# Performance work log

Hardware: AMD Instinct MI355X
Metric: run time of the kernel (lower is better)

Reference implementation:

```python
import jax, jax.numpy as jnp
import numpy as np

CUTOFF = 5.0
NIPSIN = 3
NELE = 4        # natomtype
NWAVE = 10      # ntype: radial params per element
NB, NA, NEIGH = 1, 12000, 64
NPAIR = NA * NEIGH
# index_para: maps 12 angular components (3 p + 9 d) to order index 0/1
INDEX_PARA = np.concatenate([np.full(3 ** i, i - 1, dtype=np.int32) for i in range(1, NIPSIN)])
NANG = INDEX_PARA.shape[0]  # 12


def setup_inputs() -> dict:
    key = jax.random.key(0)
    ks = jax.random.split(key, 8)
    coordinates = jax.random.normal(ks[0], (NB, NA, 3), dtype=jnp.float32)
    numatoms = NA
    atom_index = jax.random.randint(ks[1], (2, NB, NPAIR), 0, NA)
    shifts = jax.random.normal(ks[2], (NB, NPAIR, 3), dtype=jnp.float32) * 0.1
    species = jax.random.randint(ks[3], (NB * NA,), 0, NELE)
    rs = jax.random.uniform(ks[4], (NELE, NWAVE), dtype=jnp.float32) * 4.0
    inta = jax.random.uniform(ks[5], (NELE, NWAVE), dtype=jnp.float32) + 0.2
    params = jax.random.uniform(ks[6], (NELE,), dtype=jnp.float32) * 0.5 + 0.5
    return {"coordinates": coordinates, "numatoms": numatoms, "atom_index": atom_index,
            "shifts": shifts, "species": species, "rs": rs, "inta": inta, "params": params}


def _density(coordinates, atom_index, shifts, species, rs, inta):
    nb, na, _ = coordinates.shape
    coords = coordinates.reshape(-1, 3)
    totnatom = coords.shape[0]
    npair = atom_index.shape[2]
    # flatten pair index lists with per-molecule atom offset (faithful for nb=1)
    ai = jnp.transpose(atom_index, (1, 0, 2)).reshape(2, -1)                 # (2, nb*npair)
    off = jnp.broadcast_to((jnp.arange(nb) * na)[:, None], (nb, npair)).reshape(-1)
    idx12 = ai + off[None, :]
    shift_v = shifts.reshape(-1, 3)
    valid = jnp.all(shift_v > -1e9, axis=-1)                                 # padding mask (all True here)
    dist_vec = coords[idx12[0]] - coords[idx12[1]] + shift_v                 # (P,3)
    d = jnp.linalg.norm(dist_vec, axis=-1)                                   # (P,)
    sp = species[idx12[0]]                                                   # (P,)
    # radial Gaussian * cosine cutoff, params gathered per center-atom type
    fcut = 0.5 * (jnp.cos(jnp.pi * jnp.minimum(d / CUTOFF, 1.0)) + 1.0)
    radial = jnp.exp(-10.0 * inta[sp] * jnp.square(d[:, None] - rs[sp])) * fcut[:, None]
    radial = jnp.where(valid[:, None], radial, 0.0)                          # (P, NWAVE)
    # angular outer products of unit vectors: p (3) then d (9)
    u = dist_vec / d[:, None]
    orbs = []
    orb = jnp.ones((u.shape[0], 1), dtype=u.dtype)
    for _ in range(1, NIPSIN):
        orb = (orb[:, :, None] * u[:, None, :]).reshape(u.shape[0], -1)
        orbs.append(orb)
    angular = jnp.concatenate(orbs, axis=1)                                  # (P, NANG)
    # scatter-reduce into per-(atom, neighbor-type) accumulators, then square
    seg = idx12[0] * NELE + sp
    rd = jax.ops.segment_sum(radial, seg, num_segments=totnatom * NELE)
    rd = jnp.square(rd).reshape(totnatom, NELE, NWAVE)
    oa = (angular[:, :, None] * radial[:, None, :]).reshape(u.shape[0], -1)  # (P, NANG*NWAVE)
    ad = jax.ops.segment_sum(oa, seg, num_segments=totnatom * NELE)
    ad = jnp.square(ad).reshape(totnatom, NELE, NANG, NWAVE)
    # contract angular components of the same order (index_para)
    acc = jnp.zeros((totnatom, NELE, NIPSIN - 1, NWAVE), dtype=ad.dtype)
    acc = acc.at[:, :, jnp.asarray(INDEX_PARA), :].add(ad)
    return jnp.concatenate([rd, acc.reshape(totnatom, NELE, -1)], axis=2)    # (T, NELE, 30)


def reference(coordinates, numatoms, atom_index, shifts, species, rs, inta, params):
    density = _density(coordinates, atom_index, shifts, species, rs, inta)
    density_w = density * params[None, :, None]                 # einsum('ijk,j->ijk')
    g = jnp.einsum('ilj,imj->ijlm', density_w, density_w)       # (T, nfeat, NELE, NELE)
    return jnp.sqrt(g).reshape(g.shape[0], g.shape[1], -1).sum(-1)  # (T, nfeat)
```

## Files before the change

### kernel.cpp

```cpp
#include <hip/hip_runtime.h>
#include <math.h>

#define NA 12000
#define NPAIR 768000
#define NWAVE 10
#define BINS 256
#define APB 47
#define BCAP 4096
#define RCAP 3584
#define PPB 3072

__global__ __launch_bounds__(512) void bin_kernel(
        const float* __restrict__ coords,
        const int* __restrict__ ai0,
        const int* __restrict__ ai1,
        const float* __restrict__ shifts,
        unsigned int* __restrict__ cursor,
        float4* __restrict__ records,
        unsigned char* __restrict__ aloc8) {
    __shared__ unsigned int hist[BINS];
    __shared__ unsigned int scanbuf[BINS];
    __shared__ unsigned int excl[BINS];
    __shared__ unsigned int gbase[BINS];
    __shared__ float4 stage[PPB];
    __shared__ unsigned short inv[PPB];
    __shared__ unsigned int dest[PPB];

    int tid = threadIdx.x;
    if (tid < BINS) hist[tid] = 0u;
    __syncthreads();

    unsigned int binr[6], rankr[6], alocr[6];
    int pbase = blockIdx.x * PPB;
    #pragma unroll
    for (int r = 0; r < 6; r++) {
        int li = r * 512 + tid;
        int p  = pbase + li;
        int a  = ai0[p];
        int j  = ai1[p];
        float sx = shifts[3 * p + 0];
        float sy = shifts[3 * p + 1];
        float sz = shifts[3 * p + 2];
        float dx = coords[3 * a + 0] - coords[3 * j + 0] + sx;
        float dy = coords[3 * a + 1] - coords[3 * j + 1] + sy;
        float dz = coords[3 * a + 2] - coords[3 * j + 2] + sz;
        float d  = sqrtf(dx * dx + dy * dy + dz * dz);
        float tt = fminf(d * 0.2f, 1.0f);
        float fcut = 0.5f * __cosf(3.14159265358979f * tt) + 0.5f;
        if (!((sx > -1e9f) && (sy > -1e9f) && (sz > -1e9f))) fcut = 0.0f;
        unsigned int bin  = (unsigned int)a / 47u;
        unsigned int aloc = (unsigned int)a - bin * 47u;
        stage[li] = make_float4(dx, dy, dz, fcut);
        unsigned int rk = atomicAdd(&hist[bin], 1u);
        binr[r] = bin;
        rankr[r] = rk;
        alocr[r] = aloc;
    }
    __syncthreads();

    unsigned int h = (tid < BINS) ? hist[tid] : 0u;
    if (tid < BINS) scanbuf[tid] = h;
    __syncthreads();
    for (int off = 1; off < BINS; off <<= 1) {
        unsigned int v = (tid < BINS && tid >= off) ? scanbuf[tid - off] : 0u;
        __syncthreads();
        if (tid < BINS) scanbuf[tid] += v;
        __syncthreads();
    }
    if (tid < BINS) {
        excl[tid]  = scanbuf[tid] - h;
        gbase[tid] = atomicAdd(&cursor[tid], h);
    }
    __syncthreads();

    #pragma unroll
    for (int r = 0; r < 6; r++) {
        int li = r * 512 + tid;
        unsigned int s  = excl[binr[r]] + rankr[r];
        unsigned int gr = gbase[binr[r]] + rankr[r];
        inv[s]  = (unsigned short)li;
        dest[s] = (gr < BCAP) ? (binr[r] * BCAP + gr) : 0xFFFFFFFFu;
        stage[li].w = __uint_as_float((__float_as_uint(stage[li].w) & ~63u) | alocr[r]);
    }
    __syncthreads();

    #pragma unroll
    for (int r = 0; r < 6; r++) {
        int s = r * 512 + tid;
        unsigned int dg = dest[s];
        float4 rec = stage[inv[s]];
        unsigned int al = __float_as_uint(rec.w) & 63u;
        rec.w = __uint_as_float(__float_as_uint(rec.w) & ~63u);
        if (dg != 0xFFFFFFFFu) {
            records[dg] = rec;
            aloc8[dg] = (unsigned char)al;
        }
    }
}

__global__ __launch_bounds__(256) void accum_kernel(
        const float4* __restrict__ records,
        const unsigned char* __restrict__ aloc8,
        const int*    __restrict__ species,
        const float*  __restrict__ params,
        const float*  __restrict__ rs,
        const float*  __restrict__ inta,
        const unsigned int* __restrict__ cursor,
        float* __restrict__ out) {
    __shared__ unsigned short idx[RCAP];
    __shared__ float spart[4][APB * 101];
    __shared__ unsigned int hist[APB];
    __shared__ unsigned int offs[APB];
    __shared__ int spl[APB];

    int tid  = threadIdx.x;
    int wv   = tid >> 6;
    int lane = tid & 63;
    int bin  = blockIdx.x;

    if (tid < APB) {
        hist[tid] = 0u;
        int ag = bin * APB + tid;
        spl[tid] = (ag < NA) ? species[ag] : 0;
    }
    __syncthreads();

    unsigned int cnt = cursor[bin];
    if (cnt > RCAP) cnt = RCAP;
    unsigned int base = (unsigned int)bin * BCAP;

    unsigned int pend[14];
    #pragma unroll
    for (int r = 0; r < 14; r++) {
        unsigned int k = (unsigned int)(r * 256 + tid);
        pend[r] = 0xFFFFFFFFu;
        if (k < cnt) {
            unsigned int aloc = aloc8[base + k];
            unsigned int rk = atomicAdd(&hist[aloc], 1u);
            pend[r] = (aloc << 20) | (rk << 12) | k;
        }
    }
    __syncthreads();

    if (wv == 0) {
        unsigned int h0 = (lane < APB) ? hist[lane] : 0u;
        unsigned int h = h0;
        #pragma unroll
        for (int s = 1; s < 64; s <<= 1) {
            unsigned int v = __shfl_up(h, s, 64);
            if (lane >= s) h += v;
        }
        if (lane < APB) offs[lane] = h - h0;
    }
    __syncthreads();

    #pragma unroll
    for (int r = 0; r < 14; r++) {
        if (pend[r] != 0xFFFFFFFFu) {
            unsigned int aloc = pend[r] >> 20;
            unsigned int rk   = (pend[r] >> 12) & 0xFFu;
            unsigned int k    = pend[r] & 0xFFFu;
            idx[offs[aloc] + rk] = (unsigned short)k;
        }
    }
    __syncthreads();

    if (lane < APB) {
        int a = lane;
        unsigned int offa = offs[a];
        unsigned int cnta = hist[a];
        int sp = spl[a];
        float trs[10], tin[10];
        #pragma unroll
        for (int w = 0; w < 10; w++) {
            trs[w] = rs[sp * NWAVE + w];
            tin[w] = -10.0f * inta[sp * NWAVE + w];
        }

        float S[10], P[30], D[60];
        #pragma unroll
        for (int w = 0; w < 10; w++) S[w] = 0.0f;
        #pragma unroll
        for (int c = 0; c < 30; c++) P[c] = 0.0f;
        #pragma unroll
        for (int c = 0; c < 60; c++) D[c] = 0.0f;

        for (unsigned int j = (unsigned int)wv; j < cnta; j += 4) {
            unsigned int k = idx[offa + j];
            float4 rec = records[base + k];
            float fcut = rec.w;
            float d2 = rec.x * rec.x + rec.y * rec.y + rec.z * rec.z;
            float dinv = rsqrtf(fmaxf(d2, 1e-24f));
            float d  = d2 * dinv;
            float ux = rec.x * dinv, uy = rec.y * dinv, uz = rec.z * dinv;
            float uxx = ux * ux, uxy = ux * uy, uxz = ux * uz;
            float uyy = uy * uy, uyz = uy * uz, uzz = uz * uz;
            #pragma unroll
            for (int w = 0; w < 10; w++) {
                float dr = d - trs[w];
                float r  = __expf(tin[w] * dr * dr) * fcut;
                S[w]      += r;
                P[w]      += ux  * r;
                P[10 + w] += uy  * r;
                P[20 + w] += uz  * r;
                D[w]      += uxx * r;
                D[10 + w] += uxy * r;
                D[20 + w] += uxz * r;
                D[30 + w] += uyy * r;
                D[40 + w] += uyz * r;
                D[50 + w] += uzz * r;
            }
        }

        float* row = &spart[wv][a * 101];
        #pragma unroll
        for (int w = 0; w < 10; w++) row[w]      = S[w];
        #pragma unroll
        for (int c = 0; c < 30; c++) row[10 + c] = P[c];
        #pragma unroll
        for (int c = 0; c < 60; c++) row[40 + c] = D[c];
    }
    __syncthreads();

    for (int v = tid; v < APB * 30; v += 256) {
        int atom = v / 30;
        int c = v - atom * 30;
        int ag = bin * APB + atom;
        if (ag < NA) {
            float pr = params[spl[atom]];
            int ao = atom * 101;
            float o;
            if (c < 10) {
                float s = spart[0][ao+c] + spart[1][ao+c] + spart[2][ao+c] + spart[3][ao+c];
                o = pr * s * s;
            } else if (c < 20) {
                int w = ao + c;
                float a1 = spart[0][w]    + spart[1][w]    + spart[2][w]    + spart[3][w];
                float b1 = spart[0][w+10] + spart[1][w+10] + spart[2][w+10] + spart[3][w+10];
                float c1 = spart[0][w+20] + spart[1][w+20] + spart[2][w+20] + spart[3][w+20];
                o = pr * (a1 * a1 + b1 * b1 + c1 * c1);
            } else {
                int w = ao + c + 20;
                float xx = spart[0][w]    + spart[1][w]    + spart[2][w]    + spart[3][w];
                float xy = spart[0][w+10] + spart[1][w+10] + spart[2][w+10] + spart[3][w+10];
                float xz = spart[0][w+20] + spart[1][w+20] + spart[2][w+20] + spart[3][w+20];
                float yy = spart[0][w+30] + spart[1][w+30] + spart[2][w+30] + spart[3][w+30];
                float yz = spart[0][w+40] + spart[1][w+40] + spart[2][w+40] + spart[3][w+40];
                float zz = spart[0][w+50] + spart[1][w+50] + spart[2][w+50] + spart[3][w+50];
                o = pr * (xx * xx + yy * yy + zz * zz
                          + 2.0f * (xy * xy + xz * xz + yz * yz));
            }
            out[ag * 30 + c] = o;
        }
    }
}


extern "C" void kernel_launch(void* const* d_in, const int* in_sizes, int n_in,
                              void* d_out, int out_size, void* d_ws, size_t ws_size,
                              hipStream_t stream) {
    const float* coords  = (const float*)d_in[0];
    const int*   aidx    = (const int*)d_in[2];
    const float* shifts  = (const float*)d_in[3];
    const int*   species = (const int*)d_in[4];
    const float* rs      = (const float*)d_in[5];
    const float* inta    = (const float*)d_in[6];
    const float* params  = (const float*)d_in[7];
    float* out = (float*)d_out;

    char* ws = (char*)d_ws;
    float4*        records = (float4*)(ws);
    unsigned int*  cursor  = (unsigned int*)(ws + 16777216);
    unsigned char* aloc8   = (unsigned char*)(ws + 16778240);

    const int* ai0 = aidx;
    const int* ai1 = aidx + NPAIR;

    hipMemsetAsync(cursor, 0, BINS * sizeof(unsigned int), stream);
    bin_kernel<<<NPAIR / PPB, 512, 0, stream>>>(coords, ai0, ai1, shifts,
                                                cursor, records, aloc8);
    accum_kernel<<<BINS, 256, 0, stream>>>(records, aloc8, species, params,
                                           rs, inta, cursor, out);
}
```

Before: 116.5 us.

## Drop LDS staging in binning and double waves in accumulation kernel

The binning kernel no longer does a block-local prefix scan and LDS reorder. Each thread keeps its records in registers and scatters them straight to global slots from the per-bin atomic base plus its local rank. This removes several barriers and LDS traffic, but global writes become less coalesced. The accumulation kernel goes from 4 to 8 waves per block so each atom's neighbor loop is split across more waves. A separate LDS reduction pass then sums the 8 partial rows, which raises LDS usage and may lower occupancy.

```diff
diff --git a/kernel.cpp b/kernel.cpp
--- a/kernel.cpp
+++ b/kernel.cpp
@@ -19,23 +19,18 @@
         float4* __restrict__ records,
         unsigned char* __restrict__ aloc8) {
     __shared__ unsigned int hist[BINS];
-    __shared__ unsigned int scanbuf[BINS];
-    __shared__ unsigned int excl[BINS];
     __shared__ unsigned int gbase[BINS];
-    __shared__ float4 stage[PPB];
-    __shared__ unsigned short inv[PPB];
-    __shared__ unsigned int dest[PPB];
 
     int tid = threadIdx.x;
     if (tid < BINS) hist[tid] = 0u;
     __syncthreads();
 
-    unsigned int binr[6], rankr[6], alocr[6];
+    float4 recr[6];
+    unsigned int meta[6];
     int pbase = blockIdx.x * PPB;
     #pragma unroll
     for (int r = 0; r < 6; r++) {
-        int li = r * 512 + tid;
-        int p  = pbase + li;
+        int p  = pbase + r * 512 + tid;
         int a  = ai0[p];
         int j  = ai1[p];
         float sx = shifts[3 * p + 0];
@@ -50,55 +45,29 @@
         if (!((sx > -1e9f) && (sy > -1e9f) && (sz > -1e9f))) fcut = 0.0f;
         unsigned int bin  = (unsigned int)a / 47u;
         unsigned int aloc = (unsigned int)a - bin * 47u;
-        stage[li] = make_float4(dx, dy, dz, fcut);
+        recr[r] = make_float4(dx, dy, dz, fcut);
         unsigned int rk = atomicAdd(&hist[bin], 1u);
-        binr[r] = bin;
-        rankr[r] = rk;
-        alocr[r] = aloc;
-    }
-    __syncthreads();
-
-    unsigned int h = (tid < BINS) ? hist[tid] : 0u;
-    if (tid < BINS) scanbuf[tid] = h;
-    __syncthreads();
-    for (int off = 1; off < BINS; off <<= 1) {
-        unsigned int v = (tid < BINS && tid >= off) ? scanbuf[tid - off] : 0u;
-        __syncthreads();
-        if (tid < BINS) scanbuf[tid] += v;
-        __syncthreads();
-    }
-    if (tid < BINS) {
-        excl[tid]  = scanbuf[tid] - h;
-        gbase[tid] = atomicAdd(&cursor[tid], h);
-    }
+        meta[r] = (bin << 18) | (aloc << 12) | rk;
+    }
+    __syncthreads();
+
+    if (tid < BINS) gbase[tid] = atomicAdd(&cursor[tid], hist[tid]);
     __syncthreads();
 
     #pragma unroll
     for (int r = 0; r < 6; r++) {
-        int li = r * 512 + tid;
-        unsigned int s  = excl[binr[r]] + rankr[r];
-        unsigned int gr = gbase[binr[r]] + rankr[r];
-        inv[s]  = (unsigned short)li;
-        dest[s] = (gr < BCAP) ? (binr[r] * BCAP + gr) : 0xFFFFFFFFu;
-        stage[li].w = __uint_as_float((__float_as_uint(stage[li].w) & ~63u) | alocr[r]);
-    }
-    __syncthreads();
-
-    #pragma unroll
-    for (int r = 0; r < 6; r++) {
-        int s = r * 512 + tid;
-        unsigned int dg = dest[s];
-        float4 rec = stage[inv[s]];
-        unsigned int al = __float_as_uint(rec.w) & 63u;
-        rec.w = __uint_as_float(__float_as_uint(rec.w) & ~63u);
-        if (dg != 0xFFFFFFFFu) {
-            records[dg] = rec;
-            aloc8[dg] = (unsigned char)al;
+        unsigned int bin  = meta[r] >> 18;
+        unsigned int aloc = (meta[r] >> 12) & 63u;
+        unsigned int gr   = gbase[bin] + (meta[r] & 0xFFFu);
+        if (gr < BCAP) {
+            unsigned int dg = bin * BCAP + gr;
+            records[dg] = recr[r];
+            aloc8[dg] = (unsigned char)aloc;
         }
     }
 }
 
-__global__ __launch_bounds__(256) void accum_kernel(
+__global__ __launch_bounds__(512) void accum_kernel(
         const float4* __restrict__ records,
         const unsigned char* __restrict__ aloc8,
         const int*    __restrict__ species,
@@ -108,7 +77,7 @@
         const unsigned int* __restrict__ cursor,
         float* __restrict__ out) {
     __shared__ unsigned short idx[RCAP];
-    __shared__ float spart[4][APB * 101];
+    __shared__ float spart[8][APB * 101];
     __shared__ unsigned int hist[APB];
     __shared__ unsigned int offs[APB];
     __shared__ int spl[APB];
@@ -129,10 +98,10 @@
     if (cnt > RCAP) cnt = RCAP;
     unsigned int base = (unsigned int)bin * BCAP;
 
-    unsigned int pend[14];
-    #pragma unroll
-    for (int r = 0; r < 14; r++) {
-        unsigned int k = (unsigned int)(r * 256 + tid);
+    unsigned int pend[7];
+    #pragma unroll
+    for (int r = 0; r < 7; r++) {
+        unsigned int k = (unsigned int)(r * 512 + tid);
         pend[r] = 0xFFFFFFFFu;
         if (k < cnt) {
             unsigned int aloc = aloc8[base + k];
@@ -155,7 +124,7 @@
     __syncthreads();
 
     #pragma unroll
-    for (int r = 0; r < 14; r++) {
+    for (int r = 0; r < 7; r++) {
         if (pend[r] != 0xFFFFFFFFu) {
             unsigned int aloc = pend[r] >> 20;
             unsigned int rk   = (pend[r] >> 12) & 0xFFu;
@@ -185,7 +154,7 @@
         #pragma unroll
         for (int c = 0; c < 60; c++) D[c] = 0.0f;
 
-        for (unsigned int j = (unsigned int)wv; j < cnta; j += 4) {
+        for (unsigned int j = (unsigned int)wv; j < cnta; j += 8) {
             unsigned int k = idx[offa + j];
             float4 rec = records[base + k];
             float fcut = rec.w;
@@ -222,31 +191,32 @@
     }
     __syncthreads();
 
-    for (int v = tid; v < APB * 30; v += 256) {
+    for (int i = tid; i < APB * 101; i += 512) {
+        float s = spart[0][i] + spart[1][i] + spart[2][i] + spart[3][i]
+                + spart[4][i] + spart[5][i] + spart[6][i] + spart[7][i];
+        spart[0][i] = s;
+    }
+    __syncthreads();
+
+    for (int v = tid; v < APB * 30; v += 512) {
         int atom = v / 30;
         int c = v - atom * 30;
         int ag = bin * APB + atom;
         if (ag < NA) {
             float pr = params[spl[atom]];
-            int ao = atom * 101;
+            const float* ap = &spart[0][atom * 101];
             float o;
             if (c < 10) {
-                float s = spart[0][ao+c] + spart[1][ao+c] + spart[2][ao+c] + spart[3][ao+c];
+                float s = ap[c];
                 o = pr * s * s;
             } else if (c < 20) {
-                int w = ao + c;
-                float a1 = spart[0][w]    + spart[1][w]    + spart[2][w]    + spart[3][w];
-                float b1 = spart[0][w+10] + spart[1][w+10] + spart[2][w+10] + spart[3][w+10];
-                float c1 = spart[0][w+20] + spart[1][w+20] + spart[2][w+20] + spart[3][w+20];
+                int w = c - 10;
+                float a1 = ap[10 + w], b1 = ap[20 + w], c1 = ap[30 + w];
                 o = pr * (a1 * a1 + b1 * b1 + c1 * c1);
             } else {
-                int w = ao + c + 20;
-                float xx = spart[0][w]    + spart[1][w]    + spart[2][w]    + spart[3][w];
-                float xy = spart[0][w+10] + spart[1][w+10] + spart[2][w+10] + spart[3][w+10];
-                float xz = spart[0][w+20] + spart[1][w+20] + spart[2][w+20] + spart[3][w+20];
-                float yy = spart[0][w+30] + spart[1][w+30] + spart[2][w+30] + spart[3][w+30];
-                float yz = spart[0][w+40] + spart[1][w+40] + spart[2][w+40] + spart[3][w+40];
-                float zz = spart[0][w+50] + spart[1][w+50] + spart[2][w+50] + spart[3][w+50];
+                int w = c - 20;
+                float xx = ap[40 + w], xy = ap[50 + w], xz = ap[60 + w];
+                float yy = ap[70 + w], yz = ap[80 + w], zz = ap[90 + w];
                 o = pr * (xx * xx + yy * yy + zz * zz
                           + 2.0f * (xy * xy + xz * xz + yz * yz));
             }
@@ -279,6 +249,6 @@
     hipMemsetAsync(cursor, 0, BINS * sizeof(unsigned int), stream);
     bin_kernel<<<NPAIR / PPB, 512, 0, stream>>>(coords, ai0, ai1, shifts,
                                                 cursor, records, aloc8);
-    accum_kernel<<<BINS, 256, 0, stream>>>(records, aloc8, species, params,
+    accum_kernel<<<BINS, 512, 0, stream>>>(records, aloc8, species, params,
                                            rs, inta, cursor, out);
 }
```

After: 111.4 us (median of 2 runs). 4.3% less time.
